# Optimization experiments

Hardware: AMD Instinct MI355X
Metric: run time of the kernel (lower is better)

## Reference

```python
import jax, jax.numpy as jnp
import numpy as np

NUM_TOKENS = 16384
INPUT_DIM = 4096
NUM_EXPERTS = 64
TOPK = 2


def setup_inputs() -> dict:
    key = jax.random.key(0)
    k1, k2 = jax.random.split(key)
    tokens = jax.random.normal(k1, (NUM_TOKENS, INPUT_DIM), dtype=jnp.float32)
    # nn.Linear(input_dim, num_experts).weight has shape [num_experts, input_dim]
    W = jax.random.normal(k2, (NUM_EXPERTS, INPUT_DIM), dtype=jnp.float32) * (1.0 / np.sqrt(INPUT_DIM))
    return {"tokens": tokens, "W": W}


def reference(tokens, W):
    # logits: [num_tokens, num_experts] = tokens @ W.T
    logits = jnp.einsum("td,ed->te", tokens, W)
    scores = jax.nn.softmax(logits, axis=-1)
    topk_scores, topk_indices = jax.lax.top_k(scores, TOPK)
    return topk_scores, topk_indices
```

## Files before the change

### kernel.cpp

```cpp
#include <hip/hip_runtime.h>
#include <math.h>

#define NTOK 16384
#define DIM  4096
#define NEXP 64
#define KS   2
#define KSL  (DIM / KS)
#define BK   64
#define NCH  (KSL / BK)
#define BM   64

typedef __fp16 f16x8  __attribute__((ext_vector_type(8)));
typedef __fp16 f16x4  __attribute__((ext_vector_type(4)));
typedef __fp16 f16x2  __attribute__((ext_vector_type(2)));
typedef float  f32x16 __attribute__((ext_vector_type(16)));

__device__ __forceinline__ void gl_lds16(const void* g, void* l) {
  __builtin_amdgcn_global_load_lds(
      (const __attribute__((address_space(1))) void*)g,
      (__attribute__((address_space(3))) void*)l, 16, 0, 0);
}

__global__ __launch_bounds__(256) void split_w(
    const float* __restrict__ W,
    __fp16* __restrict__ Wh,
    __fp16* __restrict__ Wl)
{
  const int i = (blockIdx.x * 256 + threadIdx.x) * 4;
  const float4 w = *(const float4*)(W + i);
  f16x4 h, l;
  h[0] = (__fp16)w.x; h[1] = (__fp16)w.y; h[2] = (__fp16)w.z; h[3] = (__fp16)w.w;
  l[0] = (__fp16)(w.x - (float)h[0]);
  l[1] = (__fp16)(w.y - (float)h[1]);
  l[2] = (__fp16)(w.z - (float)h[2]);
  l[3] = (__fp16)(w.w - (float)h[3]);
  *(f16x4*)(Wh + i) = h;
  *(f16x4*)(Wl + i) = l;
}

__global__ __launch_bounds__(256, 2) void router_mfma(
    const float* __restrict__ tokens,
    const __fp16* __restrict__ Wh,
    const __fp16* __restrict__ Wl,
    float* __restrict__ partial)
{
  __shared__ float  As[2][BM * BK];
  __shared__ __fp16 Bh[2][NEXP * BK];
  __shared__ __fp16 Bl[2][NEXP * BK];

  const int tid  = threadIdx.x;
  const int wid  = tid >> 6;
  const int lane = tid & 63;
  const int rc2  = lane & 31;
  const int q2   = lane >> 5;
  const int wr   = wid >> 1;
  const int ec   = wid & 1;
  const int s    = blockIdx.x & (KS - 1);
  const int tb   = (blockIdx.x >> 1) * BM;
  const int kbase = s * KSL;

  const int l16 = lane >> 4;
  const int aj  = lane & 15;
  const float* ap0 = tokens + (size_t)(tb + 16*wid +  0 + l16) * DIM + kbase + ((aj ^ ( 0 + l16)) << 2);
  const float* ap1 = tokens + (size_t)(tb + 16*wid +  4 + l16) * DIM + kbase + ((aj ^ ( 4 + l16)) << 2);
  const float* ap2 = tokens + (size_t)(tb + 16*wid +  8 + l16) * DIM + kbase + ((aj ^ ( 8 + l16)) << 2);
  const float* ap3 = tokens + (size_t)(tb + 16*wid + 12 + l16) * DIM + kbase + ((aj ^ (12 + l16)) << 2);
  const int l8 = lane >> 3;
  const int bj = lane & 7;
  const size_t bo0 = (size_t)(16*wid + 0 + l8) * DIM + kbase + ((bj ^ l8) << 3);
  const size_t bo1 = (size_t)(16*wid + 8 + l8) * DIM + kbase + ((bj ^ l8) << 3);
  const __fp16* bh0s = Wh + bo0; const __fp16* bh1s = Wh + bo1;
  const __fp16* bl0s = Wl + bo0; const __fp16* bl1s = Wl + bo1;

#define STAGE(buf, c) {                                          \
    const int ko = (c) * BK;                                     \
    gl_lds16(ap0 + ko, &As[buf][(16 * wid +  0) * BK]);          \
    gl_lds16(ap1 + ko, &As[buf][(16 * wid +  4) * BK]);          \
    gl_lds16(ap2 + ko, &As[buf][(16 * wid +  8) * BK]);          \
    gl_lds16(ap3 + ko, &As[buf][(16 * wid + 12) * BK]);          \
    gl_lds16(bh0s + ko, &Bh[buf][(16 * wid + 0) * BK]);          \
    gl_lds16(bh1s + ko, &Bh[buf][(16 * wid + 8) * BK]);          \
    gl_lds16(bl0s + ko, &Bl[buf][(16 * wid + 0) * BK]);          \
    gl_lds16(bl1s + ko, &Bl[buf][(16 * wid + 8) * BK]);          \
  }

  f32x16 acc = {0,0,0,0, 0,0,0,0, 0,0,0,0, 0,0,0,0};

  const int akey = rc2 & 15;
  const int bkey = rc2 & 7;
  const int Arow = (32 * wr + rc2) * BK;
  const int Brow = (32 * ec + rc2) * BK;

#define KSTEP(buf, kk) {                                                     \
    const int u0 = 4 * (kk) + 2 * q2;                                        \
    const float4 a0 = *(const float4*)(&As[buf][Arow + ((u0    ) ^ akey) * 4]); \
    const float4 a1 = *(const float4*)(&As[buf][Arow + ((u0 + 1) ^ akey) * 4]); \
    const int ub = ((2 * (kk) + q2) ^ bkey) * 8;                             \
    const f16x8 bhv = *(const f16x8*)(&Bh[buf][Brow + ub]);                  \
    const f16x8 blv = *(const f16x8*)(&Bl[buf][Brow + ub]);                  \
    const f16x2 h0 = __builtin_amdgcn_cvt_pkrtz(a0.x, a0.y);                 \
    const f16x2 h1 = __builtin_amdgcn_cvt_pkrtz(a0.z, a0.w);                 \
    const f16x2 h2 = __builtin_amdgcn_cvt_pkrtz(a1.x, a1.y);                 \
    const f16x2 h3 = __builtin_amdgcn_cvt_pkrtz(a1.z, a1.w);                 \
    const f16x2 m0 = __builtin_amdgcn_cvt_pkrtz(a0.x - (float)h0[0],         \
                                                a0.y - (float)h0[1]);        \
    const f16x2 m1 = __builtin_amdgcn_cvt_pkrtz(a0.z - (float)h1[0],         \
                                                a0.w - (float)h1[1]);        \
    const f16x2 m2 = __builtin_amdgcn_cvt_pkrtz(a1.x - (float)h2[0],         \
                                                a1.y - (float)h2[1]);        \
    const f16x2 m3 = __builtin_amdgcn_cvt_pkrtz(a1.z - (float)h3[0],         \
                                                a1.w - (float)h3[1]);        \
    const f16x8 Ah = {h0[0],h0[1],h1[0],h1[1],h2[0],h2[1],h3[0],h3[1]};      \
    const f16x8 Am = {m0[0],m0[1],m1[0],m1[1],m2[0],m2[1],m3[0],m3[1]};      \
    acc = __builtin_amdgcn_mfma_f32_32x32x16_f16(Ah, bhv, acc, 0, 0, 0);     \
    acc = __builtin_amdgcn_mfma_f32_32x32x16_f16(Ah, blv, acc, 0, 0, 0);     \
    acc = __builtin_amdgcn_mfma_f32_32x32x16_f16(Am, bhv, acc, 0, 0, 0);     \
  }

#define COMP(buf) { KSTEP(buf, 0); KSTEP(buf, 1); KSTEP(buf, 2); KSTEP(buf, 3); }

  STAGE(0, 0);
  __syncthreads();

  for (int c = 0; c < NCH; c += 2) {
    if (c + 1 < NCH) STAGE(1, c + 1);
    COMP(0);
    __syncthreads();
    if (c + 2 < NCH) STAGE(0, c + 2);
    COMP(1);
    __syncthreads();
  }
#undef STAGE
#undef COMP
#undef KSTEP

  float* P = partial + ((size_t)s * NTOK + tb + 32 * wr) * NEXP + 32 * ec;
  #pragma unroll
  for (int reg = 0; reg < 16; ++reg) {
    const int row = (reg & 3) + 8 * (reg >> 2) + 4 * q2;
    P[(size_t)row * NEXP + rc2] = acc[reg];
  }
}

__global__ __launch_bounds__(64) void router_finish(
    const float* __restrict__ partial,
    float* __restrict__ out)
{
  const int t = blockIdx.x * 64 + threadIdx.x;

  float l[NEXP];
  const float* p0 = partial + (size_t)t * NEXP;
  #pragma unroll
  for (int qq = 0; qq < 16; ++qq) {
    const float4 v = *(const float4*)(p0 + qq * 4);
    l[qq*4+0] = v.x; l[qq*4+1] = v.y; l[qq*4+2] = v.z; l[qq*4+3] = v.w;
  }
  #pragma unroll
  for (int s = 1; s < KS; ++s) {
    const float* p = partial + ((size_t)s * NTOK + t) * NEXP;
    #pragma unroll
    for (int qq = 0; qq < 16; ++qq) {
      const float4 v = *(const float4*)(p + qq * 4);
      l[qq*4+0] += v.x; l[qq*4+1] += v.y; l[qq*4+2] += v.z; l[qq*4+3] += v.w;
    }
  }

  float t1v = l[0]; int t1i = 0;
  float t2v = -INFINITY; int t2i = NEXP;
  #pragma unroll
  for (int e = 1; e < NEXP; ++e) {
    const float v = l[e];
    if (v > t1v) { t2v = t1v; t2i = t1i; t1v = v; t1i = e; }
    else if (v > t2v) { t2v = v; t2i = e; }
  }

  float ssum = 0.f;
  #pragma unroll
  for (int e = 0; e < NEXP; ++e) ssum += expf(l[e] - t1v);

  const float inv = 1.0f / ssum;
  out[t * 2 + 0] = inv;
  out[t * 2 + 1] = expf(t2v - t1v) * inv;
  out[2 * NTOK + t * 2 + 0] = (float)t1i;
  out[2 * NTOK + t * 2 + 1] = (float)t2i;
}

extern "C" void kernel_launch(void* const* d_in, const int* in_sizes, int n_in,
                              void* d_out, int out_size, void* d_ws, size_t ws_size,
                              hipStream_t stream) {
  const float* tokens = (const float*)d_in[0];
  const float* W      = (const float*)d_in[1];
  float* out          = (float*)d_out;

  __fp16* Wh = (__fp16*)d_ws;
  __fp16* Wl = Wh + (size_t)NEXP * DIM;
  float* partial = (float*)((char*)d_ws + (size_t)2 * NEXP * DIM * sizeof(__fp16));

  split_w<<<(NEXP * DIM) / 1024, 256, 0, stream>>>(W, Wh, Wl);
  router_mfma<<<(NTOK / BM) * KS, 256, 0, stream>>>(tokens, Wh, Wl, partial);
  router_finish<<<NTOK / 64, 64, 0, stream>>>(partial, out);
}
```

Baseline: 70.81 us.

## Fuse split-K reduction and softmax top-k into the MFMA router kernel

Replaces the two-block split-K scheme and the separate finish kernel with one 512-thread block per 64 tokens. The two K halves are handled by two wave groups, reduced through LDS, and softmax plus top-2 are computed in the same block. This removes the global partial-logit round trip and one kernel launch. In exchange each block needs twice the LDS (about 96KB) at one block per CU, and only 64 threads do the epilogue.

```diff
diff --git a/kernel.cpp b/kernel.cpp
--- a/kernel.cpp
+++ b/kernel.cpp
@@ -4,10 +4,9 @@
 #define NTOK 16384
 #define DIM  4096
 #define NEXP 64
-#define KS   2
-#define KSL  (DIM / KS)
+#define KHL  (DIM / 2)
 #define BK   64
-#define NCH  (KSL / BK)
+#define NCH  (KHL / BK)
 #define BM   64
 
 typedef __fp16 f16x8  __attribute__((ext_vector_type(8)));
@@ -38,50 +37,51 @@
   *(f16x4*)(Wl + i) = l;
 }
 
-__global__ __launch_bounds__(256, 2) void router_mfma(
+__global__ __launch_bounds__(512, 1) void router_fused(
     const float* __restrict__ tokens,
     const __fp16* __restrict__ Wh,
     const __fp16* __restrict__ Wl,
-    float* __restrict__ partial)
+    float* __restrict__ out)
 {
-  __shared__ float  As[2][BM * BK];
-  __shared__ __fp16 Bh[2][NEXP * BK];
-  __shared__ __fp16 Bl[2][NEXP * BK];
+  __shared__ float  As[2][2][BM * BK];
+  __shared__ __fp16 Bh[2][2][NEXP * BK];
+  __shared__ __fp16 Bl[2][2][NEXP * BK];
 
   const int tid  = threadIdx.x;
   const int wid  = tid >> 6;
   const int lane = tid & 63;
+  const int kh   = wid >> 2;
+  const int gw   = wid & 3;
   const int rc2  = lane & 31;
   const int q2   = lane >> 5;
-  const int wr   = wid >> 1;
-  const int ec   = wid & 1;
-  const int s    = blockIdx.x & (KS - 1);
-  const int tb   = (blockIdx.x >> 1) * BM;
-  const int kbase = s * KSL;
+  const int wr   = gw >> 1;
+  const int ec   = gw & 1;
+  const int tb   = blockIdx.x * BM;
+  const int kbase = kh * KHL;
 
   const int l16 = lane >> 4;
   const int aj  = lane & 15;
-  const float* ap0 = tokens + (size_t)(tb + 16*wid +  0 + l16) * DIM + kbase + ((aj ^ ( 0 + l16)) << 2);
-  const float* ap1 = tokens + (size_t)(tb + 16*wid +  4 + l16) * DIM + kbase + ((aj ^ ( 4 + l16)) << 2);
-  const float* ap2 = tokens + (size_t)(tb + 16*wid +  8 + l16) * DIM + kbase + ((aj ^ ( 8 + l16)) << 2);
-  const float* ap3 = tokens + (size_t)(tb + 16*wid + 12 + l16) * DIM + kbase + ((aj ^ (12 + l16)) << 2);
+  const float* ap0 = tokens + (size_t)(tb + 16*gw +  0 + l16) * DIM + kbase + ((aj ^ ( 0 + l16)) << 2);
+  const float* ap1 = tokens + (size_t)(tb + 16*gw +  4 + l16) * DIM + kbase + ((aj ^ ( 4 + l16)) << 2);
+  const float* ap2 = tokens + (size_t)(tb + 16*gw +  8 + l16) * DIM + kbase + ((aj ^ ( 8 + l16)) << 2);
+  const float* ap3 = tokens + (size_t)(tb + 16*gw + 12 + l16) * DIM + kbase + ((aj ^ (12 + l16)) << 2);
   const int l8 = lane >> 3;
   const int bj = lane & 7;
-  const size_t bo0 = (size_t)(16*wid + 0 + l8) * DIM + kbase + ((bj ^ l8) << 3);
-  const size_t bo1 = (size_t)(16*wid + 8 + l8) * DIM + kbase + ((bj ^ l8) << 3);
+  const size_t bo0 = (size_t)(16*gw + 0 + l8) * DIM + kbase + ((bj ^ l8) << 3);
+  const size_t bo1 = (size_t)(16*gw + 8 + l8) * DIM + kbase + ((bj ^ l8) << 3);
   const __fp16* bh0s = Wh + bo0; const __fp16* bh1s = Wh + bo1;
   const __fp16* bl0s = Wl + bo0; const __fp16* bl1s = Wl + bo1;
 
 #define STAGE(buf, c) {                                          \
     const int ko = (c) * BK;                                     \
-    gl_lds16(ap0 + ko, &As[buf][(16 * wid +  0) * BK]);          \
-    gl_lds16(ap1 + ko, &As[buf][(16 * wid +  4) * BK]);          \
-    gl_lds16(ap2 + ko, &As[buf][(16 * wid +  8) * BK]);          \
-    gl_lds16(ap3 + ko, &As[buf][(16 * wid + 12) * BK]);          \
-    gl_lds16(bh0s + ko, &Bh[buf][(16 * wid + 0) * BK]);          \
-    gl_lds16(bh1s + ko, &Bh[buf][(16 * wid + 8) * BK]);          \
-    gl_lds16(bl0s + ko, &Bl[buf][(16 * wid + 0) * BK]);          \
-    gl_lds16(bl1s + ko, &Bl[buf][(16 * wid + 8) * BK]);          \
+    gl_lds16(ap0 + ko, &As[kh][buf][(16 * gw +  0) * BK]);       \
+    gl_lds16(ap1 + ko, &As[kh][buf][(16 * gw +  4) * BK]);       \
+    gl_lds16(ap2 + ko, &As[kh][buf][(16 * gw +  8) * BK]);       \
+    gl_lds16(ap3 + ko, &As[kh][buf][(16 * gw + 12) * BK]);       \
+    gl_lds16(bh0s + ko, &Bh[kh][buf][(16 * gw + 0) * BK]);       \
+    gl_lds16(bh1s + ko, &Bh[kh][buf][(16 * gw + 8) * BK]);       \
+    gl_lds16(bl0s + ko, &Bl[kh][buf][(16 * gw + 0) * BK]);       \
+    gl_lds16(bl1s + ko, &Bl[kh][buf][(16 * gw + 8) * BK]);       \
   }
 
   f32x16 acc = {0,0,0,0, 0,0,0,0, 0,0,0,0, 0,0,0,0};
@@ -93,11 +93,11 @@
 
 #define KSTEP(buf, kk) {                                                     \
     const int u0 = 4 * (kk) + 2 * q2;                                        \
-    const float4 a0 = *(const float4*)(&As[buf][Arow + ((u0    ) ^ akey) * 4]); \
-    const float4 a1 = *(const float4*)(&As[buf][Arow + ((u0 + 1) ^ akey) * 4]); \
+    const float4 a0 = *(const float4*)(&As[kh][buf][Arow + ((u0    ) ^ akey) * 4]); \
+    const float4 a1 = *(const float4*)(&As[kh][buf][Arow + ((u0 + 1) ^ akey) * 4]); \
     const int ub = ((2 * (kk) + q2) ^ bkey) * 8;                             \
-    const f16x8 bhv = *(const f16x8*)(&Bh[buf][Brow + ub]);                  \
-    const f16x8 blv = *(const f16x8*)(&Bl[buf][Brow + ub]);                  \
+    const f16x8 bhv = *(const f16x8*)(&Bh[kh][buf][Brow + ub]);              \
+    const f16x8 blv = *(const f16x8*)(&Bl[kh][buf][Brow + ub]);              \
     const f16x2 h0 = __builtin_amdgcn_cvt_pkrtz(a0.x, a0.y);                 \
     const f16x2 h1 = __builtin_amdgcn_cvt_pkrtz(a0.z, a0.w);                 \
     const f16x2 h2 = __builtin_amdgcn_cvt_pkrtz(a1.x, a1.y);                 \
@@ -134,55 +134,46 @@
 #undef COMP
 #undef KSTEP
 
-  float* P = partial + ((size_t)s * NTOK + tb + 32 * wr) * NEXP + 32 * ec;
+  float* Ls = &As[0][0][0];
   #pragma unroll
   for (int reg = 0; reg < 16; ++reg) {
     const int row = (reg & 3) + 8 * (reg >> 2) + 4 * q2;
-    P[(size_t)row * NEXP + rc2] = acc[reg];
+    if (kh == 0)
+      Ls[(32 * wr + row) * 65 + 32 * ec + rc2] = acc[reg];
   }
-}
+  __syncthreads();
+  #pragma unroll
+  for (int reg = 0; reg < 16; ++reg) {
+    const int row = (reg & 3) + 8 * (reg >> 2) + 4 * q2;
+    if (kh == 1)
+      Ls[(32 * wr + row) * 65 + 32 * ec + rc2] += acc[reg];
+  }
+  __syncthreads();
 
-__global__ __launch_bounds__(64) void router_finish(
-    const float* __restrict__ partial,
-    float* __restrict__ out)
-{
-  const int t = blockIdx.x * 64 + threadIdx.x;
+  if (tid < 64) {
+    const int t = tb + tid;
+    float l[NEXP];
+    #pragma unroll
+    for (int e = 0; e < NEXP; ++e) l[e] = Ls[tid * 65 + e];
 
-  float l[NEXP];
-  const float* p0 = partial + (size_t)t * NEXP;
-  #pragma unroll
-  for (int qq = 0; qq < 16; ++qq) {
-    const float4 v = *(const float4*)(p0 + qq * 4);
-    l[qq*4+0] = v.x; l[qq*4+1] = v.y; l[qq*4+2] = v.z; l[qq*4+3] = v.w;
+    float t1v = l[0]; int t1i = 0;
+    float t2v = -INFINITY; int t2i = NEXP;
+    #pragma unroll
+    for (int e = 1; e < NEXP; ++e) {
+      const float v = l[e];
+      if (v > t1v) { t2v = t1v; t2i = t1i; t1v = v; t1i = e; }
+      else if (v > t2v) { t2v = v; t2i = e; }
+    }
+    float ssum = 0.f;
+    #pragma unroll
+    for (int e = 0; e < NEXP; ++e) ssum += expf(l[e] - t1v);
+
+    const float inv = 1.0f / ssum;
+    out[t * 2 + 0] = inv;
+    out[t * 2 + 1] = expf(t2v - t1v) * inv;
+    out[2 * NTOK + t * 2 + 0] = (float)t1i;
+    out[2 * NTOK + t * 2 + 1] = (float)t2i;
   }
-  #pragma unroll
-  for (int s = 1; s < KS; ++s) {
-    const float* p = partial + ((size_t)s * NTOK + t) * NEXP;
-    #pragma unroll
-    for (int qq = 0; qq < 16; ++qq) {
-      const float4 v = *(const float4*)(p + qq * 4);
-      l[qq*4+0] += v.x; l[qq*4+1] += v.y; l[qq*4+2] += v.z; l[qq*4+3] += v.w;
-    }
-  }
-
-  float t1v = l[0]; int t1i = 0;
-  float t2v = -INFINITY; int t2i = NEXP;
-  #pragma unroll
-  for (int e = 1; e < NEXP; ++e) {
-    const float v = l[e];
-    if (v > t1v) { t2v = t1v; t2i = t1i; t1v = v; t1i = e; }
-    else if (v > t2v) { t2v = v; t2i = e; }
-  }
-
-  float ssum = 0.f;
-  #pragma unroll
-  for (int e = 0; e < NEXP; ++e) ssum += expf(l[e] - t1v);
-
-  const float inv = 1.0f / ssum;
-  out[t * 2 + 0] = inv;
-  out[t * 2 + 1] = expf(t2v - t1v) * inv;
-  out[2 * NTOK + t * 2 + 0] = (float)t1i;
-  out[2 * NTOK + t * 2 + 1] = (float)t2i;
 }
 
 extern "C" void kernel_launch(void* const* d_in, const int* in_sizes, int n_in,
@@ -194,9 +185,7 @@
 
   __fp16* Wh = (__fp16*)d_ws;
   __fp16* Wl = Wh + (size_t)NEXP * DIM;
-  float* partial = (float*)((char*)d_ws + (size_t)2 * NEXP * DIM * sizeof(__fp16));
 
   split_w<<<(NEXP * DIM) / 1024, 256, 0, stream>>>(W, Wh, Wl);
-  router_mfma<<<(NTOK / BM) * KS, 256, 0, stream>>>(tokens, Wh, Wl, partial);
-  router_finish<<<NTOK / 64, 64, 0, stream>>>(partial, out);
+  router_fused<<<NTOK / BM, 512, 0, stream>>>(tokens, Wh, Wl, out);
 }
```

Result: no change. 69.84 us (median of 2 runs) (-1.4%).
